# Kernel tuning notes

Measured on AMD Instinct MI355X. Metric: run time of the kernel, lower is better.

The kernel has to match this reference:

```python
import jax, jax.numpy as jnp
import numpy as np

G = 4096      # number of graphs in the batch
N = 524288    # total nodes across batch (avg 128 nodes/graph)
H = 128       # hidden_size


def setup_inputs() -> dict:
    key = jax.random.key(0)
    ks = jax.random.split(key, 8)
    s1 = 1.0 / np.sqrt(2 * H)
    s2 = 1.0 / np.sqrt(H)
    return {
        "updated_set": jax.random.normal(ks[0], (G, H), jnp.float32),
        "updated_node": jax.random.normal(ks[1], (N, H), jnp.float32),
        "segment_ids": jnp.sort(jax.random.randint(ks[2], (N,), 0, G, jnp.int32)),
        "Ws1": jax.random.normal(ks[3], (2 * H, H), jnp.float32) * s1,
        "bs1": jnp.zeros((H,), jnp.float32),
        "Ws2": jax.random.normal(ks[4], (H, H), jnp.float32) * s2,
        "bs2": jnp.zeros((H,), jnp.float32),
        "Wn1": jax.random.normal(ks[5], (2 * H, H), jnp.float32) * s1,
        "bn1": jnp.zeros((H,), jnp.float32),
        "Wn2": jax.random.normal(ks[6], (H, H), jnp.float32) * s2,
        "bn2": jnp.zeros((H,), jnp.float32),
    }


def reference(updated_set, updated_node, segment_ids, Ws1, bs1, Ws2, bs2, Wn1, bn1, Wn2, bn2):
    num_graphs = updated_set.shape[0]
    # SumPooling: segment-sum node features per graph -> [G, H]
    nodes_agg = jax.ops.segment_sum(updated_node, segment_ids, num_segments=num_graphs)
    # set update: concat([G,H],[G,H]) -> MLP 2H->H->H with ReLU
    s_in = jnp.concatenate([nodes_agg, updated_set], axis=1)
    s = jax.nn.relu(jax.nn.relu(s_in @ Ws1 + bs1) @ Ws2 + bs2)
    # tile(): broadcast each graph's set state to its nodes = gather by segment id
    n_in = jnp.concatenate([updated_node, s[segment_ids]], axis=1)  # [N, 2H]
    n = jax.nn.relu(jax.nn.relu(n_in @ Wn1 + bn1) @ Wn2 + bn2)
    return s, n
```

## Files before the change

kernel.cpp:

```cpp
#include <hip/hip_runtime.h>

#define NG 4096
#define NN 524288
#define H  128
#define H2 256

typedef __attribute__((ext_vector_type(8))) short bf16x8;
typedef __attribute__((ext_vector_type(4))) float floatx4;
typedef __attribute__((ext_vector_type(2))) unsigned int uint2v;
typedef __attribute__((ext_vector_type(4))) unsigned int uint4v;

__device__ __forceinline__ unsigned short bf16r(float f) {
    unsigned int u = __builtin_bit_cast(unsigned int, f);
    u += 0x7fffu + ((u >> 16) & 1u);
    return (unsigned short)(u >> 16);
}
__device__ __forceinline__ unsigned int bf16pk2(float a, float b) {
    return (unsigned int)bf16r(a) | ((unsigned int)bf16r(b) << 16);
}

#define SS_ROWS 256
#define SS_CH   8
#define SS_LEN  (SS_ROWS / SS_CH)

__global__ __launch_bounds__(256) void seg_sum_atomic(
    const float* __restrict__ node, const int* __restrict__ seg,
    float* __restrict__ agg) {
    const int c4   = (threadIdx.x & 31) * 4;
    const int base = blockIdx.x * SS_ROWS + (threadIdx.x >> 5) * SS_LEN;

    floatx4 acc = {0.f, 0.f, 0.f, 0.f};
    int cur = seg[base];
    #pragma unroll 4
    for (int r = 0; r < SS_LEN; ++r) {
        const int row = base + r;
        const int sgv = seg[row];
        const floatx4 v = *(const floatx4*)(node + (size_t)row * H + c4);
        if (sgv != cur) {
            float* a = &agg[(size_t)cur * H + c4];
            atomicAdd(a + 0, acc[0]); atomicAdd(a + 1, acc[1]);
            atomicAdd(a + 2, acc[2]); atomicAdd(a + 3, acc[3]);
            acc = (floatx4){0.f, 0.f, 0.f, 0.f};
            cur = sgv;
        }
        acc += v;
    }
    float* a = &agg[(size_t)cur * H + c4];
    atomicAdd(a + 0, acc[0]); atomicAdd(a + 1, acc[1]);
    atomicAdd(a + 2, acc[2]); atomicAdd(a + 3, acc[3]);
}

#define BSTR 264

template<int TILES_, bool GATHER, bool NT>
__global__ __launch_bounds__(256) void mlp_mfma(
    const float* __restrict__ in0, const int* __restrict__ seg,
    const float* __restrict__ in1,
    const float* __restrict__ W1, const float* __restrict__ b1,
    const float* __restrict__ W2, const float* __restrict__ b2,
    float* __restrict__ outp) {

    __shared__ unsigned short ldsB[2][16 * BSTR];
    __shared__ unsigned short ldsH[16 * 136];

    const int tid   = threadIdx.x;
    const int wid   = tid >> 6;
    const int lane  = tid & 63;
    const int l16   = lane & 15;
    const int quad  = lane >> 4;
    const int fbase = wid * 32;
    const int sr = tid >> 4;
    const int sc = tid & 15;

    bf16x8 A1[2][8];
    #pragma unroll
    for (int mt = 0; mt < 2; ++mt)
        #pragma unroll
        for (int kt = 0; kt < 8; ++kt) {
            const float* b = W1 + (size_t)(kt * 32 + quad * 8) * H
                                + fbase + mt * 16 + l16;
            union { unsigned int u[4]; bf16x8 v; } r;
            #pragma unroll
            for (int j = 0; j < 4; ++j)
                r.u[j] = bf16pk2(b[(2 * j) * H], b[(2 * j + 1) * H]);
            A1[mt][kt] = r.v;
        }
    bf16x8 A2[2][4];
    #pragma unroll
    for (int mt = 0; mt < 2; ++mt)
        #pragma unroll
        for (int kt = 0; kt < 4; ++kt) {
            const float* b = W2 + (size_t)(kt * 32 + quad * 8) * H
                                + fbase + mt * 16 + l16;
            union { unsigned int u[4]; bf16x8 v; } r;
            #pragma unroll
            for (int j = 0; j < 4; ++j)
                r.u[j] = bf16pk2(b[(2 * j) * H], b[(2 * j + 1) * H]);
            A2[mt][kt] = r.v;
        }
    floatx4 b1v[2], b2v[2];
    #pragma unroll
    for (int mt = 0; mt < 2; ++mt) {
        b1v[mt] = *(const floatx4*)(b1 + fbase + mt * 16 + quad * 4);
        b2v[mt] = *(const floatx4*)(b2 + fbase + mt * 16 + quad * 4);
    }

    const int nb0 = blockIdx.x * (TILES_ * 16);

    floatx4 pf[4];

    auto stage_load = [&](int t) {
        const int row = nb0 + t * 16 + sr;
        const float* p;
        if (sc < 8) {
            p = in0 + (size_t)row * H + sc * 16;
        } else {
            const int g = GATHER ? seg[row] : row;
            p = in1 + (size_t)g * H + (sc - 8) * 16;
        }
        #pragma unroll
        for (int i = 0; i < 4; ++i)
            pf[i] = *(const floatx4*)(p + i * 4);
    };
    auto stage_write = [&](int buf) {
        unsigned short* d = &ldsB[buf][sr * BSTR + sc * 16];
        uint4v w0 = (uint4v){ bf16pk2(pf[0][0], pf[0][1]), bf16pk2(pf[0][2], pf[0][3]),
                              bf16pk2(pf[1][0], pf[1][1]), bf16pk2(pf[1][2], pf[1][3]) };
        uint4v w1 = (uint4v){ bf16pk2(pf[2][0], pf[2][1]), bf16pk2(pf[2][2], pf[2][3]),
                              bf16pk2(pf[3][0], pf[3][1]), bf16pk2(pf[3][2], pf[3][3]) };
        *(uint4v*)d = w0;
        *(uint4v*)(d + 8) = w1;
    };

    stage_load(0);
    stage_write(0);

    for (int t = 0; t < TILES_; ++t) {
        __syncthreads();
        if (t + 1 < TILES_) stage_load(t + 1);

        floatx4 acc1[2];
        acc1[0] = (floatx4){0.f, 0.f, 0.f, 0.f};
        acc1[1] = (floatx4){0.f, 0.f, 0.f, 0.f};
        const unsigned short* bsrc = &ldsB[t & 1][0];
        #pragma unroll
        for (int kt = 0; kt < 8; ++kt) {
            bf16x8 bf = *(const bf16x8*)(bsrc + l16 * BSTR + kt * 32 + quad * 8);
            acc1[0] = __builtin_amdgcn_mfma_f32_16x16x32_bf16(A1[0][kt], bf, acc1[0], 0, 0, 0);
            acc1[1] = __builtin_amdgcn_mfma_f32_16x16x32_bf16(A1[1][kt], bf, acc1[1], 0, 0, 0);
        }
        #pragma unroll
        for (int mt = 0; mt < 2; ++mt) {
            floatx4 v = acc1[mt] + b1v[mt];
            uint2v u;
            u[0] = bf16pk2(fmaxf(v[0], 0.f), fmaxf(v[1], 0.f));
            u[1] = bf16pk2(fmaxf(v[2], 0.f), fmaxf(v[3], 0.f));
            *(uint2v*)&ldsH[l16 * 136 + fbase + mt * 16 + quad * 4] = u;
        }
        if (t + 1 < TILES_) stage_write((t + 1) & 1);

        __syncthreads();

        floatx4 acc2[2];
        acc2[0] = (floatx4){0.f, 0.f, 0.f, 0.f};
        acc2[1] = (floatx4){0.f, 0.f, 0.f, 0.f};
        #pragma unroll
        for (int kt = 0; kt < 4; ++kt) {
            bf16x8 bf = *(const bf16x8*)&ldsH[l16 * 136 + kt * 32 + quad * 8];
            acc2[0] = __builtin_amdgcn_mfma_f32_16x16x32_bf16(A2[0][kt], bf, acc2[0], 0, 0, 0);
            acc2[1] = __builtin_amdgcn_mfma_f32_16x16x32_bf16(A2[1][kt], bf, acc2[1], 0, 0, 0);
        }
        const int nb = nb0 + t * 16;
        #pragma unroll
        for (int mt = 0; mt < 2; ++mt) {
            floatx4 v = acc2[mt] + b2v[mt];
            floatx4 o;
            o[0] = fmaxf(v[0], 0.f); o[1] = fmaxf(v[1], 0.f);
            o[2] = fmaxf(v[2], 0.f); o[3] = fmaxf(v[3], 0.f);
            float* dst = outp + (size_t)(nb + l16) * H + fbase + mt * 16 + quad * 4;
            if (NT) __builtin_nontemporal_store(o, (floatx4*)dst);
            else    *(floatx4*)dst = o;
        }
    }
}

extern "C" void kernel_launch(void* const* d_in, const int* in_sizes, int n_in,
                              void* d_out, int out_size, void* d_ws, size_t ws_size,
                              hipStream_t stream) {
    const float* updated_set  = (const float*)d_in[0];
    const float* updated_node = (const float*)d_in[1];
    const int*   segment_ids  = (const int*)  d_in[2];
    const float* Ws1 = (const float*)d_in[3];
    const float* bs1 = (const float*)d_in[4];
    const float* Ws2 = (const float*)d_in[5];
    const float* bs2 = (const float*)d_in[6];
    const float* Wn1 = (const float*)d_in[7];
    const float* bn1 = (const float*)d_in[8];
    const float* Wn2 = (const float*)d_in[9];
    const float* bn2 = (const float*)d_in[10];

    float* s_out = (float*)d_out;
    float* n_out = (float*)d_out + (size_t)NG * H;
    float* agg   = (float*)d_ws;

    hipMemsetAsync(agg, 0, (size_t)NG * H * sizeof(float), stream);

    seg_sum_atomic<<<NN / SS_ROWS, 256, 0, stream>>>(updated_node, segment_ids, agg);

    mlp_mfma<1, false, false><<<NG / 16, 256, 0, stream>>>(
        agg, nullptr, updated_set, Ws1, bs1, Ws2, bs2, s_out);

    mlp_mfma<16, true, true><<<NN / (16 * 16), 256, 0, stream>>>(
        updated_node, segment_ids, s_out, Wn1, bn1, Wn2, bn2, n_out);
}
```

Baseline: 635.4 us.

## Deepen input prefetch to two tiles and use hardware bf16 pack conversion

After: 613.9 us. -3.4%, faster.

```diff
diff --git a/kernel.cpp b/kernel.cpp
--- a/kernel.cpp
+++ b/kernel.cpp
@@ -10,13 +10,10 @@
 typedef __attribute__((ext_vector_type(2))) unsigned int uint2v;
 typedef __attribute__((ext_vector_type(4))) unsigned int uint4v;
 
-__device__ __forceinline__ unsigned short bf16r(float f) {
-    unsigned int u = __builtin_bit_cast(unsigned int, f);
-    u += 0x7fffu + ((u >> 16) & 1u);
-    return (unsigned short)(u >> 16);
-}
-__device__ __forceinline__ unsigned int bf16pk2(float a, float b) {
-    return (unsigned int)bf16r(a) | ((unsigned int)bf16r(b) << 16);
+__device__ __forceinline__ unsigned int cvtpk2(float a, float b) {
+    unsigned int r;
+    asm("v_cvt_pk_bf16_f32 %0, %1, %2" : "=v"(r) : "v"(a), "v"(b));
+    return r;
 }
 
 #define SS_ROWS 256
@@ -69,8 +66,8 @@
     const int l16   = lane & 15;
     const int quad  = lane >> 4;
     const int fbase = wid * 32;
-    const int sr = tid >> 4;
-    const int sc = tid & 15;
+    const int sr    = tid >> 4;
+    const int sc    = tid & 15;
 
     bf16x8 A1[2][8];
     #pragma unroll
@@ -82,7 +79,7 @@
             union { unsigned int u[4]; bf16x8 v; } r;
             #pragma unroll
             for (int j = 0; j < 4; ++j)
-                r.u[j] = bf16pk2(b[(2 * j) * H], b[(2 * j + 1) * H]);
+                r.u[j] = cvtpk2(b[(2 * j) * H], b[(2 * j + 1) * H]);
             A1[mt][kt] = r.v;
         }
     bf16x8 A2[2][4];
@@ -95,7 +92,7 @@
             union { unsigned int u[4]; bf16x8 v; } r;
             #pragma unroll
             for (int j = 0; j < 4; ++j)
-                r.u[j] = bf16pk2(b[(2 * j) * H], b[(2 * j + 1) * H]);
+                r.u[j] = cvtpk2(b[(2 * j) * H], b[(2 * j + 1) * H]);
             A2[mt][kt] = r.v;
         }
     floatx4 b1v[2], b2v[2];
@@ -107,81 +104,88 @@
 
     const int nb0 = blockIdx.x * (TILES_ * 16);
 
-    floatx4 pf[4];
-
-    auto stage_load = [&](int t) {
-        const int row = nb0 + t * 16 + sr;
-        const float* p;
-        if (sc < 8) {
-            p = in0 + (size_t)row * H + sc * 16;
-        } else {
-            const int g = GATHER ? seg[row] : row;
-            p = in1 + (size_t)g * H + (sc - 8) * 16;
-        }
-        #pragma unroll
-        for (int i = 0; i < 4; ++i)
-            pf[i] = *(const floatx4*)(p + i * 4);
-    };
-    auto stage_write = [&](int buf) {
-        unsigned short* d = &ldsB[buf][sr * BSTR + sc * 16];
-        uint4v w0 = (uint4v){ bf16pk2(pf[0][0], pf[0][1]), bf16pk2(pf[0][2], pf[0][3]),
-                              bf16pk2(pf[1][0], pf[1][1]), bf16pk2(pf[1][2], pf[1][3]) };
-        uint4v w1 = (uint4v){ bf16pk2(pf[2][0], pf[2][1]), bf16pk2(pf[2][2], pf[2][3]),
-                              bf16pk2(pf[3][0], pf[3][1]), bf16pk2(pf[3][2], pf[3][3]) };
-        *(uint4v*)d = w0;
-        *(uint4v*)(d + 8) = w1;
-    };
-
-    stage_load(0);
-    stage_write(0);
-
-    for (int t = 0; t < TILES_; ++t) {
-        __syncthreads();
-        if (t + 1 < TILES_) stage_load(t + 1);
-
-        floatx4 acc1[2];
-        acc1[0] = (floatx4){0.f, 0.f, 0.f, 0.f};
-        acc1[1] = (floatx4){0.f, 0.f, 0.f, 0.f};
-        const unsigned short* bsrc = &ldsB[t & 1][0];
-        #pragma unroll
-        for (int kt = 0; kt < 8; ++kt) {
-            bf16x8 bf = *(const bf16x8*)(bsrc + l16 * BSTR + kt * 32 + quad * 8);
-            acc1[0] = __builtin_amdgcn_mfma_f32_16x16x32_bf16(A1[0][kt], bf, acc1[0], 0, 0, 0);
-            acc1[1] = __builtin_amdgcn_mfma_f32_16x16x32_bf16(A1[1][kt], bf, acc1[1], 0, 0, 0);
-        }
-        #pragma unroll
-        for (int mt = 0; mt < 2; ++mt) {
-            floatx4 v = acc1[mt] + b1v[mt];
-            uint2v u;
-            u[0] = bf16pk2(fmaxf(v[0], 0.f), fmaxf(v[1], 0.f));
-            u[1] = bf16pk2(fmaxf(v[2], 0.f), fmaxf(v[3], 0.f));
-            *(uint2v*)&ldsH[l16 * 136 + fbase + mt * 16 + quad * 4] = u;
-        }
-        if (t + 1 < TILES_) stage_write((t + 1) & 1);
-
-        __syncthreads();
-
-        floatx4 acc2[2];
-        acc2[0] = (floatx4){0.f, 0.f, 0.f, 0.f};
-        acc2[1] = (floatx4){0.f, 0.f, 0.f, 0.f};
-        #pragma unroll
-        for (int kt = 0; kt < 4; ++kt) {
-            bf16x8 bf = *(const bf16x8*)&ldsH[l16 * 136 + kt * 32 + quad * 8];
-            acc2[0] = __builtin_amdgcn_mfma_f32_16x16x32_bf16(A2[0][kt], bf, acc2[0], 0, 0, 0);
-            acc2[1] = __builtin_amdgcn_mfma_f32_16x16x32_bf16(A2[1][kt], bf, acc2[1], 0, 0, 0);
-        }
-        const int nb = nb0 + t * 16;
-        #pragma unroll
-        for (int mt = 0; mt < 2; ++mt) {
-            floatx4 v = acc2[mt] + b2v[mt];
-            floatx4 o;
-            o[0] = fmaxf(v[0], 0.f); o[1] = fmaxf(v[1], 0.f);
-            o[2] = fmaxf(v[2], 0.f); o[3] = fmaxf(v[3], 0.f);
-            float* dst = outp + (size_t)(nb + l16) * H + fbase + mt * 16 + quad * 4;
-            if (NT) __builtin_nontemporal_store(o, (floatx4*)dst);
-            else    *(floatx4*)dst = o;
-        }
+    floatx4 pfA[4], pfB[4];
+
+#define STAGE_LOAD(T, PF) do {                                                \
+    const int row_ = nb0 + (T) * 16 + sr;                                     \
+    const float* p0_ = in0 + (size_t)row_ * H + sc * 8;                       \
+    PF[0] = *(const floatx4*)(p0_);                                           \
+    PF[1] = *(const floatx4*)(p0_ + 4);                                       \
+    const int g_ = GATHER ? seg[row_] : row_;                                 \
+    const float* p1_ = in1 + (size_t)g_ * H + sc * 8;                         \
+    PF[2] = *(const floatx4*)(p1_);                                           \
+    PF[3] = *(const floatx4*)(p1_ + 4);                                       \
+} while (0)
+
+#define STAGE_WRITE(BUF, PF) do {                                             \
+    unsigned short* d_ = &ldsB[BUF][sr * BSTR + sc * 8];                      \
+    *(uint4v*)d_ = (uint4v){ cvtpk2(PF[0][0], PF[0][1]),                      \
+                             cvtpk2(PF[0][2], PF[0][3]),                      \
+                             cvtpk2(PF[1][0], PF[1][1]),                      \
+                             cvtpk2(PF[1][2], PF[1][3]) };                    \
+    *(uint4v*)(d_ + 128) = (uint4v){ cvtpk2(PF[2][0], PF[2][1]),              \
+                                     cvtpk2(PF[2][2], PF[2][3]),              \
+                                     cvtpk2(PF[3][0], PF[3][1]),              \
+                                     cvtpk2(PF[3][2], PF[3][3]) };            \
+} while (0)
+
+#define TILE_BODY(T, PFW, PFL) do {                                           \
+    __syncthreads();   \
+    if ((T) + 1 < TILES_) STAGE_WRITE(((T) + 1) & 1, PFW);                    \
+    if ((T) + 2 < TILES_) STAGE_LOAD((T) + 2, PFL);                           \
+    floatx4 acc1[2];                                                          \
+    acc1[0] = (floatx4){0.f, 0.f, 0.f, 0.f};                                  \
+    acc1[1] = (floatx4){0.f, 0.f, 0.f, 0.f};                                  \
+    const unsigned short* bsrc_ = &ldsB[(T) & 1][0];                          \
+    _Pragma("unroll")                                                         \
+    for (int kt = 0; kt < 8; ++kt) {                                          \
+        bf16x8 bf = *(const bf16x8*)(bsrc_ + l16 * BSTR + kt * 32 + quad * 8);\
+        acc1[0] = __builtin_amdgcn_mfma_f32_16x16x32_bf16(A1[0][kt], bf, acc1[0], 0, 0, 0); \
+        acc1[1] = __builtin_amdgcn_mfma_f32_16x16x32_bf16(A1[1][kt], bf, acc1[1], 0, 0, 0); \
+    }                                                                         \
+    _Pragma("unroll")                                                         \
+    for (int mt = 0; mt < 2; ++mt) {                                          \
+        floatx4 v = acc1[mt] + b1v[mt];                                       \
+        uint2v u;                                                             \
+        u[0] = cvtpk2(fmaxf(v[0], 0.f), fmaxf(v[1], 0.f));                    \
+        u[1] = cvtpk2(fmaxf(v[2], 0.f), fmaxf(v[3], 0.f));                    \
+        *(uint2v*)&ldsH[l16 * 136 + fbase + mt * 16 + quad * 4] = u;          \
+    }                                                                         \
+    __syncthreads();                                        \
+    floatx4 acc2[2];                                                          \
+    acc2[0] = (floatx4){0.f, 0.f, 0.f, 0.f};                                  \
+    acc2[1] = (floatx4){0.f, 0.f, 0.f, 0.f};                                  \
+    _Pragma("unroll")                                                         \
+    for (int kt = 0; kt < 4; ++kt) {                                          \
+        bf16x8 bf = *(const bf16x8*)&ldsH[l16 * 136 + kt * 32 + quad * 8];    \
+        acc2[0] = __builtin_amdgcn_mfma_f32_16x16x32_bf16(A2[0][kt], bf, acc2[0], 0, 0, 0); \
+        acc2[1] = __builtin_amdgcn_mfma_f32_16x16x32_bf16(A2[1][kt], bf, acc2[1], 0, 0, 0); \
+    }                                                                         \
+    const int nb_ = nb0 + (T) * 16;                                           \
+    _Pragma("unroll")                                                         \
+    for (int mt = 0; mt < 2; ++mt) {                                          \
+        floatx4 v = acc2[mt] + b2v[mt];                                       \
+        floatx4 o;                                                            \
+        o[0] = fmaxf(v[0], 0.f); o[1] = fmaxf(v[1], 0.f);                     \
+        o[2] = fmaxf(v[2], 0.f); o[3] = fmaxf(v[3], 0.f);                     \
+        float* dst_ = outp + (size_t)(nb_ + l16) * H + fbase + mt * 16 + quad * 4; \
+        if (NT) __builtin_nontemporal_store(o, (floatx4*)dst_);               \
+        else    *(floatx4*)dst_ = o;                                          \
+    }                                                                         \
+} while (0)
+
+    STAGE_LOAD(0, pfA);
+    STAGE_WRITE(0, pfA);
+    if (TILES_ > 1) STAGE_LOAD(1, pfB);
+
+    for (int t = 0; t < TILES_; t += 2) {
+        TILE_BODY(t, pfB, pfA);
+        if (t + 1 < TILES_) TILE_BODY(t + 1, pfA, pfB);
     }
+
+#undef STAGE_LOAD
+#undef STAGE_WRITE
+#undef TILE_BODY
 }
 
 extern "C" void kernel_launch(void* const* d_in, const int* in_sizes, int n_in,
@@ -210,6 +214,6 @@
     mlp_mfma<1, false, false><<<NG / 16, 256, 0, stream>>>(
         agg, nullptr, updated_set, Ws1, bs1, Ws2, bs2, s_out);
 
-    mlp_mfma<16, true, true><<<NN / (16 * 16), 256, 0, stream>>>(
+    mlp_mfma<16, true, false><<<NN / (16 * 16), 256, 0, stream>>>(
         updated_node, segment_ids, s_out, Wn1, bn1, Wn2, bn2, n_out);
 }
```
